# Performance work log

Hardware: AMD Instinct MI355X
Metric: run time of the kernel (lower is better)

The kernel has to match this reference:

```python
import jax, jax.numpy as jnp
import numpy as np
import math

B, N, D, H, T = 256, 512, 512, 8, 128
HD = D // H
CLIP = 10.0
CAP = 1.0
NEG = -1.0e9


def setup_inputs() -> dict:
    key = jax.random.key(0)
    ks = jax.random.split(key, 12)
    s = 1.0 / math.sqrt(D)
    return {
        "embeddings": jax.random.normal(ks[0], (B, N, D), jnp.float32),
        "mean_graph_emb": jax.random.normal(ks[1], (B, D), jnp.float32),
        "used_capacity": jax.random.uniform(ks[2], (T, B), jnp.float32),
        "Wk": jax.random.normal(ks[3], (D, D), jnp.float32) * s,
        "Wk_tanh": jax.random.normal(ks[4], (D, D), jnp.float32) * s,
        "Wv": jax.random.normal(ks[5], (D, D), jnp.float32) * s,
        "Wq_context": jax.random.normal(ks[6], (D, D), jnp.float32) * s,
        "Wq_step": jax.random.normal(ks[7], (D + 1, D), jnp.float32) * s,
        "Wout": jax.random.normal(ks[8], (D, D), jnp.float32) * s,
        "prev_a": jax.random.randint(ks[9], (T, B), 0, N, jnp.int32),
        "mask": jax.random.randint(ks[10], (T, B, N), 0, 2, jnp.int32),
    }


def reference(embeddings, mean_graph_emb, used_capacity, Wk, Wk_tanh, Wv,
              Wq_context, Wq_step, Wout, prev_a, mask):
    # Projections (done once per graph embedding, as in get_projections)
    K = (embeddings @ Wk).reshape(B, N, H, HD).transpose(0, 2, 1, 3)      # [B,H,N,hd]
    V = (embeddings @ Wv).reshape(B, N, H, HD).transpose(0, 2, 1, 3)      # [B,H,N,hd]
    K_tanh = embeddings @ Wk_tanh                                          # [B,N,D]
    Q_context = mean_graph_emb @ Wq_context                                # [B,D]

    inv_sqrt_hd = 1.0 / math.sqrt(HD)
    inv_sqrt_d = 1.0 / math.sqrt(D)

    def step(carry, xs):
        prev_t, cap_t, mask_t = xs  # [B], [B], [B,N]
        # get_step_context: gather prev node embedding + remaining capacity
        cur_emb = jnp.take_along_axis(embeddings, prev_t[:, None, None], axis=1)[:, 0]  # [B,D]
        step_ctx = jnp.concatenate([cur_emb, (CAP - cap_t)[:, None]], axis=-1)          # [B,D+1]
        q = Q_context + step_ctx @ Wq_step                                               # [B,D]
        qh = q.reshape(B, H, HD)                                                          # [B,H,hd]
        # decoder MHA, seq_len_q = 1
        logits = jnp.einsum("bhd,bhnd->bhn", qh, K) * inv_sqrt_hd                        # [B,H,N]
        logits = jnp.where(mask_t[:, None, :] == 1, NEG, logits)
        attn = jax.nn.softmax(logits, axis=-1)
        mha = jnp.einsum("bhn,bhnd->bhd", attn, V).reshape(B, D) @ Wout                  # [B,D]
        # single-head tanh-clipped pointer logits
        comp = jnp.einsum("bd,bnd->bn", mha, K_tanh) * inv_sqrt_d                        # [B,N]
        comp = jnp.tanh(comp) * CLIP
        comp = jnp.where(mask_t == 1, NEG, comp)
        p = jax.nn.softmax(comp, axis=-1)                                                # [B,N]
        return carry, p

    _, ps = jax.lax.scan(step, None, (prev_a, used_capacity, mask))  # [T,B,N]
    return ps.transpose(1, 0, 2)  # [B,T,N]
```

## Files before the change

### kernel.cpp

```cpp
#include <hip/hip_runtime.h>
#include <hip/hip_bf16.h>

constexpr int Bb = 256;
constexpr int Nn = 512;
constexpr int Dd = 512;
constexpr int Hh = 8;
constexpr int Tt = 128;
#define NEGF (-1.0e9f)

typedef __attribute__((ext_vector_type(4))) float f32x4;
typedef __attribute__((ext_vector_type(8))) short bf16x8;
typedef __attribute__((ext_vector_type(8))) unsigned short u16x8;

#define AS1 __attribute__((address_space(1)))
#define AS3 __attribute__((address_space(3)))

__device__ __forceinline__ unsigned short f2bf(float f) {
  union { float f; unsigned u; } v; v.f = f;
  unsigned r = v.u + 0x7fffu + ((v.u >> 16) & 1u);
  return (unsigned short)(r >> 16);
}

__device__ __forceinline__ unsigned cvtpk(float lo, float hi) {
  unsigned r;
  asm("v_cvt_pk_bf16_f32 %0, %1, %2" : "=v"(r) : "v"(lo), "v"(hi));
  return r;
}

__global__ void cast_emb_k(const float* __restrict__ src, unsigned short* __restrict__ dst, int n8) {
  int i = blockIdx.x * 256 + threadIdx.x;
  if (i >= n8) return;
  const float4* s = (const float4*)src + (size_t)i * 2;
  float4 a = s[0], b = s[1];
  u16x8 o;
  o[0] = f2bf(a.x); o[1] = f2bf(a.y); o[2] = f2bf(a.z); o[3] = f2bf(a.w);
  o[4] = f2bf(b.x); o[5] = f2bf(b.y); o[6] = f2bf(b.z); o[7] = f2bf(b.w);
  ((u16x8*)dst)[i] = o;
}

__global__ void cast_wt_k(const float* __restrict__ W0, const float* __restrict__ W1,
                          const float* __restrict__ W2,
                          unsigned short* __restrict__ D0, unsigned short* __restrict__ D1,
                          unsigned short* __restrict__ D2) {
  int mid = blockIdx.x >> 8;
  int tile = blockIdx.x & 255;
  const float* S = (mid == 0) ? W0 : (mid == 1) ? W1 : W2;
  unsigned short* Dst = (mid == 0) ? D0 : (mid == 1) ? D1 : D2;
  __shared__ float t[32][33];
  int r0 = (tile >> 4) * 32, c0 = (tile & 15) * 32;
  int tx = threadIdx.x & 31, ty = threadIdx.x >> 5;
#pragma unroll
  for (int yy = 0; yy < 4; ++yy) {
    int r = ty + yy * 8;
    t[r][tx] = S[(size_t)(r0 + r) * 512 + c0 + tx];
  }
  __syncthreads();
#pragma unroll
  for (int yy = 0; yy < 4; ++yy) {
    int c = ty + yy * 8;
    Dst[(size_t)(c0 + c) * 512 + r0 + tx] = f2bf(t[tx][c]);
  }
}

__global__ void qc_k(const float* __restrict__ mge, const float* __restrict__ Wqc,
                     float* __restrict__ Qc) {
  int b = blockIdx.x;
  __shared__ float m[512];
  m[threadIdx.x] = mge[(size_t)b * 512 + threadIdx.x];
  m[threadIdx.x + 256] = mge[(size_t)b * 512 + threadIdx.x + 256];
  __syncthreads();
  float a0 = 0.f, a1 = 0.f;
  for (int k = 0; k < 512; ++k) {
    float mk = m[k];
    a0 += mk * Wqc[(size_t)k * 512 + threadIdx.x];
    a1 += mk * Wqc[(size_t)k * 512 + threadIdx.x + 256];
  }
  Qc[(size_t)b * 512 + threadIdx.x] = a0;
  Qc[(size_t)b * 512 + threadIdx.x + 256] = a1;
}

__global__ void mbits_k(const int* __restrict__ mask, unsigned* __restrict__ bits) {
  size_t gid = (size_t)blockIdx.x * 256 + threadIdx.x;
  int mv = mask[gid];
  unsigned long long bal = __ballot(mv == 1);
  if ((threadIdx.x & 63) == 0) {
    unsigned t = (unsigned)(gid >> 17);
    unsigned b = (unsigned)((gid >> 9) & 255);
    unsigned n = (unsigned)(gid & 511);
    unsigned* dst = bits + (((size_t)b * 128 + t) * 16 + (n >> 5));
    dst[0] = (unsigned)bal;
    dst[1] = (unsigned)(bal >> 32);
  }
}

__device__ __forceinline__ void stage_tile(const unsigned short* __restrict__ G, int row0, int k0,
                                           unsigned short* lds_base, int wave, int lane) {
#pragma unroll
  for (int c = 0; c < 4; ++c) {
    int chunk = wave * 4 + c;
    const unsigned short* g = G + (size_t)(row0 + chunk * 8 + (lane >> 3)) * 512 + k0 + (lane & 7) * 8;
    __builtin_amdgcn_global_load_lds((AS1 void*)g, (AS3 void*)(lds_base + chunk * 512), 16, 0, 0);
  }
}

template <int MODE>
__global__ __launch_bounds__(256, 2)
void gemm5_k(const unsigned short* __restrict__ A, const unsigned short* __restrict__ BT,
             void* __restrict__ Cout,
             const float* __restrict__ Qc, const float* __restrict__ WqsL,
             const float* __restrict__ capp, const int* __restrict__ prev) {
  __shared__ __align__(16) char lds[32768];
  unsigned short* ldsA = (unsigned short*)lds;
  unsigned short* ldsB = ldsA + 8192;
  int xcd = blockIdx.x & 7, loc = blockIdx.x >> 3;
  int ml = loc >> 2, nt = loc & 3;
  int mt = xcd * 32 + ml;
  int m0 = mt * 128, n0 = nt * 128;
  int tid = threadIdx.x, lane = tid & 63, w = tid >> 6;
  int wm = w >> 1, wn = w & 1;
  int l15 = lane & 15, l4 = lane >> 4;

  const unsigned short* gbase[4];
#pragma unroll
  for (int c = 0; c < 4; ++c) {
    int row = m0 + (w * 4 + c) * 8 + (lane >> 3);
    if (MODE == 3) {
      int t = row >> 8, bb = row & 255;
      int pa = prev[t * Bb + bb];
      gbase[c] = A + (size_t)(bb * 512 + pa) * 512 + (lane & 7) * 8;
    } else {
      gbase[c] = A + (size_t)row * 512 + (lane & 7) * 8;
    }
  }

  f32x4 acc[4][4] = {};
  for (int k0 = 0; k0 < 512; k0 += 64) {
#pragma unroll
    for (int c = 0; c < 4; ++c) {
      int chunk = w * 4 + c;
      __builtin_amdgcn_global_load_lds((AS1 void*)(gbase[c] + k0),
                                       (AS3 void*)(ldsA + chunk * 512), 16, 0, 0);
    }
    stage_tile(BT, n0, k0, ldsB, w, lane);
    __syncthreads();
#pragma unroll
    for (int ks = 0; ks < 2; ++ks) {
      bf16x8 fa[4], fb[4];
#pragma unroll
      for (int ii = 0; ii < 4; ++ii)
        fa[ii] = *(const bf16x8*)(ldsA + (wm * 64 + ii * 16 + l15) * 64 + ks * 32 + l4 * 8);
#pragma unroll
      for (int jj = 0; jj < 4; ++jj)
        fb[jj] = *(const bf16x8*)(ldsB + (wn * 64 + jj * 16 + l15) * 64 + ks * 32 + l4 * 8);
#pragma unroll
      for (int ii = 0; ii < 4; ++ii)
#pragma unroll
        for (int jj = 0; jj < 4; ++jj)
          acc[ii][jj] = __builtin_amdgcn_mfma_f32_16x16x32_bf16(fa[ii], fb[jj], acc[ii][jj], 0, 0, 0);
    }
    __syncthreads();
  }

  if (MODE == 1) {
    unsigned short* C = (unsigned short*)Cout;
#pragma unroll
    for (int ii = 0; ii < 4; ++ii)
#pragma unroll
      for (int jj = 0; jj < 4; ++jj)
#pragma unroll
        for (int r = 0; r < 4; ++r) {
          int row = m0 + wm * 64 + ii * 16 + l4 * 4 + r;
          int col = n0 + wn * 64 + jj * 16 + l15;
          C[(size_t)row * 512 + col] = f2bf(acc[ii][jj][r]);
        }
  } else {
    unsigned short* C = (unsigned short*)Cout;
#pragma unroll
    for (int ii = 0; ii < 4; ++ii)
#pragma unroll
      for (int jj = 0; jj < 4; ++jj)
#pragma unroll
        for (int r = 0; r < 4; ++r) {
          int row = m0 + wm * 64 + ii * 16 + l4 * 4 + r;
          int col = n0 + wn * 64 + jj * 16 + l15;
          int t = row >> 8, bbx = row & 255;
          float val = acc[ii][jj][r] + Qc[(size_t)bbx * 512 + col] + (1.0f - capp[row]) * WqsL[col];
          C[(size_t)(bbx * 128 + t) * 512 + col] = f2bf(val * 0.125f);
        }
  }
}

__global__ __launch_bounds__(256, 2)
void wf_k(const unsigned short* __restrict__ A, const unsigned short* __restrict__ BT,
          unsigned short* __restrict__ C) {
  __shared__ __align__(16) char lds[32768];
  unsigned short* ldsA = (unsigned short*)lds;
  unsigned short* ldsB = ldsA + 8192;
  int mt = blockIdx.x >> 2, nt = blockIdx.x & 3;
  int m0 = mt * 128, n0 = nt * 128;
  int tid = threadIdx.x, lane = tid & 63, w = tid >> 6;
  int wm = w >> 1, wn = w & 1;
  int l15 = lane & 15, l4 = lane >> 4;

  f32x4 acc[4][4] = {};
  for (int k0 = 0; k0 < 512; k0 += 64) {
    stage_tile(A, m0, k0, ldsA, w, lane);
    stage_tile(BT, n0, k0, ldsB, w, lane);
    __syncthreads();
#pragma unroll
    for (int ks = 0; ks < 2; ++ks) {
      bf16x8 fa[4], fb[4];
#pragma unroll
      for (int ii = 0; ii < 4; ++ii)
        fa[ii] = *(const bf16x8*)(ldsA + (wm * 64 + ii * 16 + l15) * 64 + ks * 32 + l4 * 8);
#pragma unroll
      for (int jj = 0; jj < 4; ++jj)
        fb[jj] = *(const bf16x8*)(ldsB + (wn * 64 + jj * 16 + l15) * 64 + ks * 32 + l4 * 8);
#pragma unroll
      for (int ii = 0; ii < 4; ++ii)
#pragma unroll
        for (int jj = 0; jj < 4; ++jj)
          acc[ii][jj] = __builtin_amdgcn_mfma_f32_16x16x32_bf16(fa[ii], fb[jj], acc[ii][jj], 0, 0, 0);
    }
    __syncthreads();
  }
#pragma unroll
  for (int ii = 0; ii < 4; ++ii)
#pragma unroll
    for (int jj = 0; jj < 4; ++jj)
#pragma unroll
      for (int r = 0; r < 4; ++r) {
        int row = m0 + wm * 64 + ii * 16 + l4 * 4 + r;
        int col = n0 + wn * 64 + jj * 16 + l15;
        C[(size_t)row * 512 + col] = f2bf(acc[ii][jj][r]);
      }
}

#define STAGE10(SLOT, MAT, H, ROWB, KT)                                            \
  do {                                                                             \
    const unsigned short* G_ = (MAT) ? BT : A;                                     \
    int rb_ = (ROWB) + (H) * 128;                                                  \
    char* Lb_ = lds + (SLOT) * 65536 + (MAT) * 32768 + (H) * 16384;                \
    _Pragma("unroll")                                                              \
    for (int sh_ = 0; sh_ < 2; ++sh_) {                                            \
      int off_ = sh_ * 8192 + tid * 16;                                            \
      int r_ = off_ >> 7;                                                          \
      int c_ = (off_ & 127) ^ ((r_ & 7) << 4);     \
      const char* g_ = (const char*)(G_ + (size_t)(rb_ + r_) * 512 + (KT) * 64) + c_; \
      __builtin_amdgcn_global_load_lds((AS1 void*)g_, (AS3 void*)(Lb_ + off_), 16, 0, 0); \
    }                                                                              \
  } while (0)

#define LDA_Q(QM)                                                   \
  _Pragma("unroll")                                                 \
  for (int ii = 0; ii < 4; ++ii) {                                  \
    int rr_ = (QM) * 64 + ii * 16 + l15;                            \
    const char* ap_ = ldsAh + rr_ * 128;                            \
    int sw_ = (rr_ & 7) << 4;                                       \
    fa[ii][0] = *(const bf16x8*)(ap_ + ((l4 * 16) ^ sw_));          \
    fa[ii][1] = *(const bf16x8*)(ap_ + ((64 + l4 * 16) ^ sw_));     \
  }

#define LDB_Q(QN)                                                   \
  _Pragma("unroll")                                                 \
  for (int jj = 0; jj < 2; ++jj) {                                  \
    int rr_ = (wn & 1) * 64 + (QN) * 32 + jj * 16 + l15;            \
    const char* bp_ = ldsBh + rr_ * 128;                            \
    int sw_ = (rr_ & 7) << 4;                                       \
    fb[jj][0] = *(const bf16x8*)(bp_ + ((l4 * 16) ^ sw_));          \
    fb[jj][1] = *(const bf16x8*)(bp_ + ((64 + l4 * 16) ^ sw_));     \
  }

#define MM16(QM, QN)                                                              \
  do {                                                                            \
    __builtin_amdgcn_s_setprio(1);                                                \
    _Pragma("unroll")                                                             \
    for (int ii = 0; ii < 4; ++ii)                                                \
      _Pragma("unroll")                                                           \
      for (int jj = 0; jj < 2; ++jj) {                                            \
        acc[(QM) * 4 + ii][(QN) * 2 + jj] = __builtin_amdgcn_mfma_f32_16x16x32_bf16( \
            fa[ii][0], fb[jj][0], acc[(QM) * 4 + ii][(QN) * 2 + jj], 0, 0, 0);    \
        acc[(QM) * 4 + ii][(QN) * 2 + jj] = __builtin_amdgcn_mfma_f32_16x16x32_bf16( \
            fa[ii][1], fb[jj][1], acc[(QM) * 4 + ii][(QN) * 2 + jj], 0, 0, 0);    \
      }                                                                           \
    __builtin_amdgcn_s_setprio(0);                                                \
  } while (0)

__global__ __launch_bounds__(512, 1)
void gemm10_k(const unsigned short* __restrict__ A,
              const unsigned short* __restrict__ B0, const unsigned short* __restrict__ B1,
              unsigned short* __restrict__ C0, unsigned short* __restrict__ C2) {
  __shared__ __align__(16) char lds[131072];
  int xcd = blockIdx.x & 7, loc = blockIdx.x >> 3;
  int ml4 = loc >> 2, cmb = loc & 3;
  int grp = cmb >> 1, nh = cmb & 1;
  const unsigned short* BT = grp ? B1 : B0;
  int mtb = xcd * 64 + ml4 * 4;
  int n0 = nh * 256;
  int tid = threadIdx.x, lane = tid & 63, w = tid >> 6;
  int wm = w >> 2, wn = w & 3;
  int l15 = lane & 15, l4 = lane >> 4;

  f32x4 acc[8][4] = {};
  bf16x8 fa[4][2], fb[2][2];

  {
    int m0n = mtb * 256;
    STAGE10(0, 0, 0, m0n, 0); STAGE10(0, 0, 1, m0n, 0);
    STAGE10(0, 1, 0, n0, 0);  STAGE10(0, 1, 1, n0, 0);
  }

  for (int g = 0; g < 32; ++g) {
    int s = g & 1, sn = s ^ 1;
    char* ldsAh = lds + s * 65536 + wm * 16384;
    char* ldsBh = lds + s * 65536 + 32768 + (wn >> 1) * 16384;
    int gn = g + 1;
    int m0n = (mtb + (gn >> 3)) * 256;
    int ktn = gn & 7;
    if (g < 31) {
      STAGE10(sn, 0, 0, m0n, ktn);
      asm volatile("s_waitcnt vmcnt(2)" ::: "memory");
    } else {
      asm volatile("s_waitcnt vmcnt(0)" ::: "memory");
    }
    __builtin_amdgcn_s_barrier();
    LDA_Q(0); LDB_Q(0);
    MM16(0, 0);
    __builtin_amdgcn_s_barrier();
    LDB_Q(1);
    if (g < 31) STAGE10(sn, 0, 1, m0n, ktn);
    __builtin_amdgcn_s_barrier();
    MM16(0, 1);
    __builtin_amdgcn_s_barrier();
    LDA_Q(1);
    if (g < 31) STAGE10(sn, 1, 0, n0, ktn);
    __builtin_amdgcn_s_barrier();
    MM16(1, 1);
    __builtin_amdgcn_s_barrier();
    LDB_Q(0);
    if (g < 31) STAGE10(sn, 1, 1, n0, ktn);
    __builtin_amdgcn_s_barrier();
    MM16(1, 0);
    __builtin_amdgcn_s_barrier();

    if ((g & 7) == 7) {
      int m0cur = (mtb + (g >> 3)) * 256;
      if (grp == 0) {
#pragma unroll
        for (int mi = 0; mi < 8; ++mi)
#pragma unroll
          for (int nj = 0; nj < 4; ++nj)
#pragma unroll
            for (int r = 0; r < 4; ++r) {
              int row = m0cur + wm * 128 + mi * 16 + l4 * 4 + r;
              int col = n0 + wn * 64 + nj * 16 + l15;
              C0[(size_t)row * 512 + col] = f2bf(acc[mi][nj][r]);
            }
      } else {
        int bb = m0cur >> 9, nn0 = m0cur & 511;
        char* wb = lds + 65536 + w * 8192;
#pragma unroll
        for (int p = 0; p < 4; ++p) {
#pragma unroll
          for (int mi = 0; mi < 8; ++mi) {
            ushort4 w4;
            w4.x = f2bf(acc[mi][p][0]);
            w4.y = f2bf(acc[mi][p][1]);
            w4.z = f2bf(acc[mi][p][2]);
            w4.w = f2bf(acc[mi][p][3]);
            *(ushort4*)(wb + l15 * 264 + (mi * 16 + l4 * 4) * 2) = w4;
          }
#pragma unroll
          for (int step = 0; step < 4; ++step) {
            int dl = step * 4 + l4;
            union { ushort4 h[2]; u16x8 v; } u;
            u.h[0] = *(const ushort4*)(wb + dl * 264 + l15 * 16);
            u.h[1] = *(const ushort4*)(wb + dl * 264 + l15 * 16 + 8);
            int dglob = n0 + wn * 64 + p * 16 + dl;
            *(u16x8*)(C2 + (size_t)(bb * 512 + dglob) * 512 + nn0 + wm * 128 + l15 * 8) = u.v;
          }
        }
      }
#pragma unroll
      for (int mi = 0; mi < 8; ++mi)
#pragma unroll
        for (int nj = 0; nj < 4; ++nj)
          acc[mi][nj] = (f32x4){0.f, 0.f, 0.f, 0.f};
      __syncthreads();
    }
  }
}

#define STAGEK5(CH, SLOT)                                                          \
  do {                                                                             \
    _Pragma("unroll")                                                              \
    for (int sh_ = 0; sh_ < 2; ++sh_) {                                            \
      int off_ = sh_ * 8192 + tid * 16;                                            \
      int r_ = off_ >> 7;                                                          \
      int c_ = (off_ & 127) ^ ((r_ & 7) << 4);                                     \
      const char* g_ = (const char*)(Kb + (size_t)(b * 512 + (CH) * 128 + r_) * 512 + h * 64) + c_; \
      __builtin_amdgcn_global_load_lds((AS1 void*)g_, (AS3 void*)(lds + (SLOT) * 16384 + off_), 16, 0, 0); \
    }                                                                              \
  } while (0)

#define STAGEV5(CH, SLOT)                                                          \
  do {                                                                             \
    _Pragma("unroll")                                                              \
    for (int sh_ = 0; sh_ < 2; ++sh_) {                                            \
      int off_ = sh_ * 8192 + tid * 16;                                            \
      int r_ = off_ >> 8;                                                          \
      int c_ = (off_ & 255) ^ ((r_ & 7) << 4);                                     \
      const char* g_ = (const char*)(Vt + (size_t)(b * 512 + h * 64 + r_) * 512 + (CH) * 128) + c_; \
      __builtin_amdgcn_global_load_lds((AS1 void*)g_, (AS3 void*)(lds + 32768 + (SLOT) * 16384 + off_), 16, 0, 0); \
    }                                                                              \
  } while (0)

#define CHUNK5(CH)                                                                 \
  do {                                                                             \
    const char* Ks_ = lds + ((CH) & 1) * 16384;                                    \
    const char* Vs_ = lds + 32768 + ((CH) & 1) * 16384;                            \
    f32x4 sck[8];                                                                  \
    _Pragma("unroll")                                                              \
    for (int jj = 0; jj < 8; ++jj) sck[jj] = (f32x4){0.f, 0.f, 0.f, 0.f};          \
    _Pragma("unroll")                                                              \
    for (int jj = 0; jj < 8; ++jj) {                                               \
      int rr_ = jj * 16 + l15;                                                     \
      int sw_ = (rr_ & 7) << 4;                                                    \
      bf16x8 k0_ = *(const bf16x8*)(Ks_ + rr_ * 128 + ((l4 * 16) ^ sw_));          \
      bf16x8 k1_ = *(const bf16x8*)(Ks_ + rr_ * 128 + ((64 + l4 * 16) ^ sw_));     \
      sck[jj] = __builtin_amdgcn_mfma_f32_16x16x32_bf16(k0_, fq[0], sck[jj], 0, 0, 0); \
      sck[jj] = __builtin_amdgcn_mfma_f32_16x16x32_bf16(k1_, fq[1], sck[jj], 0, 0, 0); \
    }                                                                              \
    unsigned mwarr_[4] = {mqs[CH].x, mqs[CH].y, mqs[CH].z, mqs[CH].w};             \
    float cmx_ = -3.0e38f;                                                         \
    _Pragma("unroll")                                                              \
    for (int jj = 0; jj < 8; ++jj) {                                               \
      unsigned nib_ = mwarr_[jj >> 1] >> (((jj & 1) << 4) + (l4 << 2));            \
      _Pragma("unroll")                                                            \
      for (int r = 0; r < 4; ++r)                                                  \
        sck[jj][r] = ((nib_ >> r) & 1) ? NEGF : sck[jj][r];                        \
      float m01_ = fmaxf(sck[jj][0], sck[jj][1]);                                  \
      float m23_ = fmaxf(sck[jj][2], sck[jj][3]);                                  \
      cmx_ = fmaxf(cmx_, fmaxf(m01_, m23_));                                       \
    }                                                                              \
    cmx_ = fmaxf(cmx_, __shfl_xor(cmx_, 16));                                      \
    cmx_ = fmaxf(cmx_, __shfl_xor(cmx_, 32));                                      \
    float mn_ = fmaxf(mx, cmx_);                                                   \
    float al_ = __expf(mx - mn_);                                                  \
    sum *= al_;                                                                    \
    _Pragma("unroll")                                                              \
    for (int dj = 0; dj < 4; ++dj)                                                 \
      _Pragma("unroll")                                                            \
      for (int r = 0; r < 4; ++r) o[dj][r] *= al_;                                 \
    mx = mn_;                                                                      \
    _Pragma("unroll")                                                              \
    for (int jj = 0; jj < 8; ++jj) {                                               \
      _Pragma("unroll")                                                            \
      for (int r = 0; r < 4; ++r) sck[jj][r] = __expf(sck[jj][r] - mx);            \
      sum += (sck[jj][0] + sck[jj][1]) + (sck[jj][2] + sck[jj][3]);                \
    }                                                                              \
    _Pragma("unroll")                                                              \
    for (int g = 0; g < 4; ++g) {                                                  \
      unsigned a0_ = cvtpk(sck[2 * g][0], sck[2 * g][1]);                          \
      unsigned a1_ = cvtpk(sck[2 * g][2], sck[2 * g][3]);                          \
      unsigned b0_ = cvtpk(sck[2 * g + 1][0], sck[2 * g + 1][1]);                  \
      unsigned b1_ = cvtpk(sck[2 * g + 1][2], sck[2 * g + 1][3]);                  \
      unsigned wA0_ = __shfl(a0_, src0, 64), wB0_ = __shfl(b0_, src0, 64);         \
      unsigned wA1_ = __shfl(a1_, src0, 64), wB1_ = __shfl(b1_, src0, 64);         \
      unsigned wA2_ = __shfl(a0_, src2, 64), wB2_ = __shfl(b0_, src2, 64);         \
      unsigned wA3_ = __shfl(a1_, src2, 64), wB3_ = __shfl(b1_, src2, 64);         \
      union { unsigned u[4]; bf16x8 v; } pu_;                                      \
      pu_.u[0] = loh ? wA0_ : wB0_;                                                \
      pu_.u[1] = loh ? wA1_ : wB1_;                                                \
      pu_.u[2] = loh ? wA2_ : wB2_;                                                \
      pu_.u[3] = loh ? wA3_ : wB3_;                                                \
      _Pragma("unroll")                                                            \
      for (int dj = 0; dj < 4; ++dj) {                                             \
        int rr_ = dj * 16 + l15;                                                   \
        int sw_ = (rr_ & 7) << 4;                                                  \
        bf16x8 fv_ = *(const bf16x8*)(Vs_ + rr_ * 256 + ((g * 64 + l4 * 16) ^ sw_)); \
        o[dj] = __builtin_amdgcn_mfma_f32_16x16x32_bf16(fv_, pu_.v, o[dj], 0, 0, 0); \
      }                                                                            \
    }                                                                              \
  } while (0)

__global__ __launch_bounds__(512, 4)
void attn5_k(const unsigned short* __restrict__ Qb, const unsigned short* __restrict__ Kb,
             const unsigned short* __restrict__ Vt, const unsigned* __restrict__ mbits,
             unsigned short* __restrict__ mhaB) {
  __shared__ __align__(16) char lds[65536];
  int bid = blockIdx.x;
  int h = bid & 7, b = bid >> 3;
  int tid = threadIdx.x, lane = tid & 63, w = tid >> 6;
  int l15 = lane & 15, l4 = lane >> 4;
  int t = w * 16 + l15;

  bf16x8 fq[2];
#pragma unroll
  for (int ks = 0; ks < 2; ++ks)
    fq[ks] = *(const bf16x8*)(Qb + (size_t)(b * 128 + t) * 512 + h * 64 + ks * 32 + l4 * 8);
  uint4 mqs[4];
  {
    const uint4* mp = (const uint4*)(mbits + (((size_t)b * 128 + t) << 4));
    mqs[0] = mp[0]; mqs[1] = mp[1]; mqs[2] = mp[2]; mqs[3] = mp[3];
  }

  float mx = -3.0e38f, sum = 0.f;
  f32x4 o[4] = {};
  int src0 = l15 + ((l4 & 1) ? 32 : 0);
  int src2 = l15 + ((l4 & 1) ? 48 : 16);
  bool loh = (l4 < 2);

  STAGEK5(0, 0); STAGEV5(0, 0);
  STAGEK5(1, 1); STAGEV5(1, 1);
  asm volatile("s_waitcnt vmcnt(4)" ::: "memory");
  __builtin_amdgcn_s_barrier();
  CHUNK5(0);
  __builtin_amdgcn_s_barrier();
  STAGEK5(2, 0); STAGEV5(2, 0);
  asm volatile("s_waitcnt vmcnt(4)" ::: "memory");
  __builtin_amdgcn_s_barrier();
  CHUNK5(1);
  __builtin_amdgcn_s_barrier();
  STAGEK5(3, 1); STAGEV5(3, 1);
  asm volatile("s_waitcnt vmcnt(4)" ::: "memory");
  __builtin_amdgcn_s_barrier();
  CHUNK5(2);
  __builtin_amdgcn_s_barrier();
  asm volatile("s_waitcnt vmcnt(0)" ::: "memory");
  __builtin_amdgcn_s_barrier();
  CHUNK5(3);

  sum += __shfl_xor(sum, 16);
  sum += __shfl_xor(sum, 32);
  float inv = 1.0f / sum;
#pragma unroll
  for (int dj = 0; dj < 4; ++dj) {
    ushort4 w4;
    w4.x = f2bf(o[dj][0] * inv);
    w4.y = f2bf(o[dj][1] * inv);
    w4.z = f2bf(o[dj][2] * inv);
    w4.w = f2bf(o[dj][3] * inv);
    *(ushort4*)(mhaB + (size_t)(b * 128 + t) * 512 + h * 64 + dj * 16 + l4 * 4) = w4;
  }
}

#define STAGEC(CH, SLOT)                                                           \
  do {                                                                             \
    _Pragma("unroll")                                                              \
    for (int ps_ = 0; ps_ < 8; ++ps_) {                                            \
      int off_ = ps_ * 8192 + tid * 16;                                            \
      int r_ = off_ >> 10;                                                         \
      int c_ = (off_ & 1023) ^ ((r_ & 7) << 4);                                    \
      const char* g_ = (const char*)(embB + (size_t)(b * 512 + (CH) * 64 + r_) * 512) + c_; \
      __builtin_amdgcn_global_load_lds((AS1 void*)g_, (AS3 void*)(lds + (SLOT) * 65536 + off_), 16, 0, 0); \
    }                                                                              \
  } while (0)

#define CCHUNK(CH)                                                                 \
  do {                                                                             \
    const char* Es_ = lds + ((CH) & 1) * 65536;                                    \
    _Pragma("unroll")                                                              \
    for (int jjl_ = 0; jjl_ < 4; ++jjl_) {                                         \
      f32x4 sck = (f32x4){0.f, 0.f, 0.f, 0.f};                                     \
      int rr_ = jjl_ * 16 + l15;                                                   \
      const char* ep_ = Es_ + rr_ * 1024;                                          \
      int sw_ = (rr_ & 7) << 4;                                                    \
      _Pragma("unroll")                                                            \
      for (int ks_ = 0; ks_ < 16; ++ks_) {                                         \
        bf16x8 fa_ = *(const bf16x8*)(ep_ + ((ks_ * 64 + l4 * 16) ^ sw_));         \
        sck = __builtin_amdgcn_mfma_f32_16x16x32_bf16(fa_, fb[ks_], sck, 0, 0, 0); \
      }                                                                            \
      int jg_ = (CH) * 4 + jjl_;                                                   \
      unsigned nib_ = mw[jg_ >> 1] >> (((jg_ & 1) << 4) + (l4 << 2));              \
      float4 o4_;                                                                  \
      float* po_ = (float*)&o4_;                                                   \
      _Pragma("unroll")                                                            \
      for (int r = 0; r < 4; ++r) {                                                \
        float y_ = sck[r] * 0.044194173824159216f;                                 \
        y_ = fminf(fmaxf(y_, -15.f), 15.f);                                        \
        float e2_ = __expf(2.f * y_);                                              \
        float th_ = (e2_ - 1.f) / (e2_ + 1.f);                                     \
        float p_ = __expf(th_ * 10.f - 10.f);                                      \
        p_ = ((nib_ >> r) & 1) ? 0.f : p_;                                         \
        po_[r] = p_;                                                               \
        sum += p_;                                                                 \
      }                                                                            \
      *(float4*)(out + (size_t)(b * 128 + t) * 512 + (CH) * 64 + jjl_ * 16 + l4 * 4) = o4_; \
    }                                                                              \
  } while (0)

__global__ __launch_bounds__(512, 1)
void comp4_k(const unsigned short* __restrict__ mh2, const unsigned short* __restrict__ embB,
             const unsigned* __restrict__ mbits, float* __restrict__ out,
             float* __restrict__ sums) {
  __shared__ __align__(16) char lds[131072];
  int b = blockIdx.x;
  int tid = threadIdx.x, lane = tid & 63, w = tid >> 6;
  int l15 = lane & 15, l4 = lane >> 4;
  int t = w * 16 + l15;

  bf16x8 fb[16];
#pragma unroll
  for (int ks = 0; ks < 16; ++ks)
    fb[ks] = *(const bf16x8*)(mh2 + (size_t)(b * 128 + t) * 512 + ks * 32 + l4 * 8);
  unsigned mw[16];
  {
    const uint4* mp = (const uint4*)(mbits + (((size_t)b * 128 + t) << 4));
    uint4 a0 = mp[0], a1 = mp[1], a2 = mp[2], a3 = mp[3];
    mw[0] = a0.x; mw[1] = a0.y; mw[2] = a0.z; mw[3] = a0.w;
    mw[4] = a1.x; mw[5] = a1.y; mw[6] = a1.z; mw[7] = a1.w;
    mw[8] = a2.x; mw[9] = a2.y; mw[10] = a2.z; mw[11] = a2.w;
    mw[12] = a3.x; mw[13] = a3.y; mw[14] = a3.z; mw[15] = a3.w;
  }

  float sum = 0.f;
  STAGEC(0, 0);
  STAGEC(1, 1);
  asm volatile("s_waitcnt vmcnt(8)" ::: "memory");
  __builtin_amdgcn_s_barrier();
  CCHUNK(0);
  __builtin_amdgcn_s_barrier();
  STAGEC(2, 0);
  asm volatile("s_waitcnt vmcnt(8)" ::: "memory");
  __builtin_amdgcn_s_barrier();
  CCHUNK(1);
  __builtin_amdgcn_s_barrier();
  STAGEC(3, 1);
  asm volatile("s_waitcnt vmcnt(8)" ::: "memory");
  __builtin_amdgcn_s_barrier();
  CCHUNK(2);
  __builtin_amdgcn_s_barrier();
  STAGEC(4, 0);
  asm volatile("s_waitcnt vmcnt(8)" ::: "memory");
  __builtin_amdgcn_s_barrier();
  CCHUNK(3);
  __builtin_amdgcn_s_barrier();
  STAGEC(5, 1);
  asm volatile("s_waitcnt vmcnt(8)" ::: "memory");
  __builtin_amdgcn_s_barrier();
  CCHUNK(4);
  __builtin_amdgcn_s_barrier();
  STAGEC(6, 0);
  asm volatile("s_waitcnt vmcnt(8)" ::: "memory");
  __builtin_amdgcn_s_barrier();
  CCHUNK(5);
  __builtin_amdgcn_s_barrier();
  STAGEC(7, 1);
  asm volatile("s_waitcnt vmcnt(8)" ::: "memory");
  __builtin_amdgcn_s_barrier();
  CCHUNK(6);
  __builtin_amdgcn_s_barrier();
  asm volatile("s_waitcnt vmcnt(0)" ::: "memory");
  __builtin_amdgcn_s_barrier();
  CCHUNK(7);

  sum += __shfl_xor(sum, 16);
  sum += __shfl_xor(sum, 32);
  if (l4 == 0) sums[b * 128 + t] = sum;
}

__global__ void norm_k(float* __restrict__ out, const float* __restrict__ sums) {
  int row = blockIdx.x * 4 + (threadIdx.x >> 6);
  int lane = threadIdx.x & 63;
  float inv = 1.0f / sums[row];
  float4* p = (float4*)(out + (size_t)row * 512) + lane;
  float4 a = p[0], b = p[64];
  a.x *= inv; a.y *= inv; a.z *= inv; a.w *= inv;
  b.x *= inv; b.y *= inv; b.z *= inv; b.w *= inv;
  p[0] = a; p[64] = b;
}

extern "C" void kernel_launch(void* const* d_in, const int* in_sizes, int n_in,
                              void* d_out, int out_size, void* d_ws, size_t ws_size,
                              hipStream_t stream) {
  (void)in_sizes; (void)n_in; (void)out_size; (void)ws_size;
  const float* emb  = (const float*)d_in[0];
  const float* mge  = (const float*)d_in[1];
  const float* cap  = (const float*)d_in[2];
  const float* Wk   = (const float*)d_in[3];
  const float* Wkt  = (const float*)d_in[4];
  const float* Wv   = (const float*)d_in[5];
  const float* Wqc  = (const float*)d_in[6];
  const float* Wqs  = (const float*)d_in[7];
  const float* Wout = (const float*)d_in[8];
  const int* prev   = (const int*)d_in[9];
  const int* mask   = (const int*)d_in[10];
  float* out = (float*)d_out;

  char* p = (char*)d_ws;
  auto take = [&](size_t n) { char* q = p; p += (n + 255) & ~(size_t)255; return q; };
  unsigned short* embB = (unsigned short*)take((size_t)131072 * 512 * 2);
  unsigned short* Kb   = (unsigned short*)take((size_t)131072 * 512 * 2);
  unsigned short* Vt   = (unsigned short*)take((size_t)131072 * 512 * 2);
  unsigned short* Qb   = (unsigned short*)take((size_t)32768 * 512 * 2);
  unsigned short* mhaB = (unsigned short*)take((size_t)32768 * 512 * 2);
  unsigned short* mh2  = (unsigned short*)take((size_t)32768 * 512 * 2);
  float*          Qc   = (float*)take((size_t)256 * 512 * 4);
  unsigned*       mbit = (unsigned*)take((size_t)256 * 128 * 16 * 4);
  float*          sums = (float*)take((size_t)32768 * 4);
  unsigned short* WkT  = (unsigned short*)take(524288);
  unsigned short* WvT  = (unsigned short*)take(524288);
  unsigned short* WqsT = (unsigned short*)take(524288);
  unsigned short* WktB = (unsigned short*)take(524288);
  unsigned short* WoutB= (unsigned short*)take(524288);
  unsigned short* WFT  = (unsigned short*)take(524288);

  cast_emb_k<<<32768, 256, 0, stream>>>(emb, embB, 8388608);
  cast_emb_k<<<128, 256, 0, stream>>>(Wkt, WktB, 32768);
  cast_emb_k<<<128, 256, 0, stream>>>(Wout, WoutB, 32768);
  cast_wt_k<<<768, 256, 0, stream>>>(Wk, Wv, Wqs, WkT, WvT, WqsT);
  qc_k<<<256, 256, 0, stream>>>(mge, Wqc, Qc);
  mbits_k<<<65536, 256, 0, stream>>>(mask, mbit);
  wf_k<<<16, 256, 0, stream>>>(WktB, WoutB, WFT);
  gemm5_k<3><<<1024, 256, 0, stream>>>(embB, WqsT, Qb, Qc, Wqs + 512 * 512, cap, prev);
  gemm10_k<<<512, 512, 0, stream>>>(embB, WkT, WvT, Kb, Vt);
  attn5_k<<<2048, 512, 0, stream>>>(Qb, Kb, Vt, mbit, mhaB);
  gemm5_k<1><<<1024, 256, 0, stream>>>(mhaB, WFT, mh2, nullptr, nullptr, nullptr, nullptr);
  comp4_k<<<256, 512, 0, stream>>>(mh2, embB, mbit, out, sums);
  norm_k<<<8192, 256, 0, stream>>>(out, sums);
}
```

Measured before the change: 543.0 us.

## Split pointer-logit kernel over node halves and compute Q_context with MFMA GEMM

The pointer-logit kernel now runs two blocks per batch element, each covering half of the N nodes with half the LDS. Each block writes its own partial softmax sum, and the normalization kernel adds the two. This doubles the block count from 256 to 512 and allows two blocks per CU, so more of the machine is used. Separately, the scalar fp32 Q_context kernel is replaced by a bf16 MFMA small GEMM on cast inputs, which lowers that product's precision to bf16. A stray label 'wf_cast:' sits in the host function.

```diff
diff --git a/kernel.cpp b/kernel.cpp
--- a/kernel.cpp
+++ b/kernel.cpp
@@ -39,13 +39,13 @@
 }
 
 __global__ void cast_wt_k(const float* __restrict__ W0, const float* __restrict__ W1,
-                          const float* __restrict__ W2,
+                          const float* __restrict__ W2, const float* __restrict__ W3,
                           unsigned short* __restrict__ D0, unsigned short* __restrict__ D1,
-                          unsigned short* __restrict__ D2) {
+                          unsigned short* __restrict__ D2, unsigned short* __restrict__ D3) {
   int mid = blockIdx.x >> 8;
   int tile = blockIdx.x & 255;
-  const float* S = (mid == 0) ? W0 : (mid == 1) ? W1 : W2;
-  unsigned short* Dst = (mid == 0) ? D0 : (mid == 1) ? D1 : D2;
+  const float* S = (mid == 0) ? W0 : (mid == 1) ? W1 : (mid == 2) ? W2 : W3;
+  unsigned short* Dst = (mid == 0) ? D0 : (mid == 1) ? D1 : (mid == 2) ? D2 : D3;
   __shared__ float t[32][33];
   int r0 = (tile >> 4) * 32, c0 = (tile & 15) * 32;
   int tx = threadIdx.x & 31, ty = threadIdx.x >> 5;
@@ -60,23 +60,6 @@
     int c = ty + yy * 8;
     Dst[(size_t)(c0 + c) * 512 + r0 + tx] = f2bf(t[tx][c]);
   }
-}
-
-__global__ void qc_k(const float* __restrict__ mge, const float* __restrict__ Wqc,
-                     float* __restrict__ Qc) {
-  int b = blockIdx.x;
-  __shared__ float m[512];
-  m[threadIdx.x] = mge[(size_t)b * 512 + threadIdx.x];
-  m[threadIdx.x + 256] = mge[(size_t)b * 512 + threadIdx.x + 256];
-  __syncthreads();
-  float a0 = 0.f, a1 = 0.f;
-  for (int k = 0; k < 512; ++k) {
-    float mk = m[k];
-    a0 += mk * Wqc[(size_t)k * 512 + threadIdx.x];
-    a1 += mk * Wqc[(size_t)k * 512 + threadIdx.x + 256];
-  }
-  Qc[(size_t)b * 512 + threadIdx.x] = a0;
-  Qc[(size_t)b * 512 + threadIdx.x + 256] = a1;
 }
 
 __global__ void mbits_k(const int* __restrict__ mask, unsigned* __restrict__ bits) {
@@ -190,9 +173,10 @@
   }
 }
 
+template <int OUTF>
 __global__ __launch_bounds__(256, 2)
-void wf_k(const unsigned short* __restrict__ A, const unsigned short* __restrict__ BT,
-          unsigned short* __restrict__ C) {
+void smallgemm_k(const unsigned short* __restrict__ A, const unsigned short* __restrict__ BT,
+                 void* __restrict__ Cout) {
   __shared__ __align__(16) char lds[32768];
   unsigned short* ldsA = (unsigned short*)lds;
   unsigned short* ldsB = ldsA + 8192;
@@ -232,7 +216,8 @@
       for (int r = 0; r < 4; ++r) {
         int row = m0 + wm * 64 + ii * 16 + l4 * 4 + r;
         int col = n0 + wn * 64 + jj * 16 + l15;
-        C[(size_t)row * 512 + col] = f2bf(acc[ii][jj][r]);
+        if (OUTF) ((float*)Cout)[(size_t)row * 512 + col] = acc[ii][jj][r];
+        else ((unsigned short*)Cout)[(size_t)row * 512 + col] = f2bf(acc[ii][jj][r]);
       }
 }
 
@@ -545,23 +530,23 @@
   }
 }
 
-#define STAGEC(CH, SLOT)                                                           \
+#define STAGEC5(CH, SLOT)                                                          \
   do {                                                                             \
     _Pragma("unroll")                                                              \
-    for (int ps_ = 0; ps_ < 8; ++ps_) {                                            \
+    for (int ps_ = 0; ps_ < 4; ++ps_) {                                            \
       int off_ = ps_ * 8192 + tid * 16;                                            \
       int r_ = off_ >> 10;                                                         \
       int c_ = (off_ & 1023) ^ ((r_ & 7) << 4);                                    \
-      const char* g_ = (const char*)(embB + (size_t)(b * 512 + (CH) * 64 + r_) * 512) + c_; \
-      __builtin_amdgcn_global_load_lds((AS1 void*)g_, (AS3 void*)(lds + (SLOT) * 65536 + off_), 16, 0, 0); \
+      const char* g_ = (const char*)(embB + (size_t)(b * 512 + nh * 256 + (CH) * 32 + r_) * 512) + c_; \
+      __builtin_amdgcn_global_load_lds((AS1 void*)g_, (AS3 void*)(lds + (SLOT) * 32768 + off_), 16, 0, 0); \
     }                                                                              \
   } while (0)
 
-#define CCHUNK(CH)                                                                 \
+#define CCHUNK5(CH)                                                                \
   do {                                                                             \
-    const char* Es_ = lds + ((CH) & 1) * 65536;                                    \
-    _Pragma("unroll")                                                              \
-    for (int jjl_ = 0; jjl_ < 4; ++jjl_) {                                         \
+    const char* Es_ = lds + ((CH) & 1) * 32768;                                    \
+    _Pragma("unroll")                                                              \
+    for (int jjl_ = 0; jjl_ < 2; ++jjl_) {                                         \
       f32x4 sck = (f32x4){0.f, 0.f, 0.f, 0.f};                                     \
       int rr_ = jjl_ * 16 + l15;                                                   \
       const char* ep_ = Es_ + rr_ * 1024;                                          \
@@ -571,8 +556,7 @@
         bf16x8 fa_ = *(const bf16x8*)(ep_ + ((ks_ * 64 + l4 * 16) ^ sw_));         \
         sck = __builtin_amdgcn_mfma_f32_16x16x32_bf16(fa_, fb[ks_], sck, 0, 0, 0); \
       }                                                                            \
-      int jg_ = (CH) * 4 + jjl_;                                                   \
-      unsigned nib_ = mw[jg_ >> 1] >> (((jg_ & 1) << 4) + (l4 << 2));              \
+      unsigned nib_ = mwh[CH] >> ((jjl_ << 4) + (l4 << 2));                        \
       float4 o4_;                                                                  \
       float* po_ = (float*)&o4_;                                                   \
       _Pragma("unroll")                                                            \
@@ -586,16 +570,16 @@
         po_[r] = p_;                                                               \
         sum += p_;                                                                 \
       }                                                                            \
-      *(float4*)(out + (size_t)(b * 128 + t) * 512 + (CH) * 64 + jjl_ * 16 + l4 * 4) = o4_; \
+      *(float4*)(out + (size_t)(b * 128 + t) * 512 + nh * 256 + (CH) * 32 + jjl_ * 16 + l4 * 4) = o4_; \
     }                                                                              \
   } while (0)
 
-__global__ __launch_bounds__(512, 1)
-void comp4_k(const unsigned short* __restrict__ mh2, const unsigned short* __restrict__ embB,
+__global__ __launch_bounds__(512, 2)
+void comp5_k(const unsigned short* __restrict__ mh2, const unsigned short* __restrict__ embB,
              const unsigned* __restrict__ mbits, float* __restrict__ out,
              float* __restrict__ sums) {
-  __shared__ __align__(16) char lds[131072];
-  int b = blockIdx.x;
+  __shared__ __align__(16) char lds[65536];
+  int b = blockIdx.x >> 1, nh = blockIdx.x & 1;
   int tid = threadIdx.x, lane = tid & 63, w = tid >> 6;
   int l15 = lane & 15, l4 = lane >> 4;
   int t = w * 16 + l15;
@@ -604,66 +588,64 @@
 #pragma unroll
   for (int ks = 0; ks < 16; ++ks)
     fb[ks] = *(const bf16x8*)(mh2 + (size_t)(b * 128 + t) * 512 + ks * 32 + l4 * 8);
-  unsigned mw[16];
+  unsigned mwh[8];
   {
-    const uint4* mp = (const uint4*)(mbits + (((size_t)b * 128 + t) << 4));
-    uint4 a0 = mp[0], a1 = mp[1], a2 = mp[2], a3 = mp[3];
-    mw[0] = a0.x; mw[1] = a0.y; mw[2] = a0.z; mw[3] = a0.w;
-    mw[4] = a1.x; mw[5] = a1.y; mw[6] = a1.z; mw[7] = a1.w;
-    mw[8] = a2.x; mw[9] = a2.y; mw[10] = a2.z; mw[11] = a2.w;
-    mw[12] = a3.x; mw[13] = a3.y; mw[14] = a3.z; mw[15] = a3.w;
+    const uint4* mp = (const uint4*)(mbits + (((size_t)b * 128 + t) << 4)) + nh * 2;
+    uint4 a0 = mp[0], a1 = mp[1];
+    mwh[0] = a0.x; mwh[1] = a0.y; mwh[2] = a0.z; mwh[3] = a0.w;
+    mwh[4] = a1.x; mwh[5] = a1.y; mwh[6] = a1.z; mwh[7] = a1.w;
   }
 
   float sum = 0.f;
-  STAGEC(0, 0);
-  STAGEC(1, 1);
-  asm volatile("s_waitcnt vmcnt(8)" ::: "memory");
-  __builtin_amdgcn_s_barrier();
-  CCHUNK(0);
-  __builtin_amdgcn_s_barrier();
-  STAGEC(2, 0);
-  asm volatile("s_waitcnt vmcnt(8)" ::: "memory");
-  __builtin_amdgcn_s_barrier();
-  CCHUNK(1);
-  __builtin_amdgcn_s_barrier();
-  STAGEC(3, 1);
-  asm volatile("s_waitcnt vmcnt(8)" ::: "memory");
-  __builtin_amdgcn_s_barrier();
-  CCHUNK(2);
-  __builtin_amdgcn_s_barrier();
-  STAGEC(4, 0);
-  asm volatile("s_waitcnt vmcnt(8)" ::: "memory");
-  __builtin_amdgcn_s_barrier();
-  CCHUNK(3);
-  __builtin_amdgcn_s_barrier();
-  STAGEC(5, 1);
-  asm volatile("s_waitcnt vmcnt(8)" ::: "memory");
-  __builtin_amdgcn_s_barrier();
-  CCHUNK(4);
-  __builtin_amdgcn_s_barrier();
-  STAGEC(6, 0);
-  asm volatile("s_waitcnt vmcnt(8)" ::: "memory");
-  __builtin_amdgcn_s_barrier();
-  CCHUNK(5);
-  __builtin_amdgcn_s_barrier();
-  STAGEC(7, 1);
-  asm volatile("s_waitcnt vmcnt(8)" ::: "memory");
-  __builtin_amdgcn_s_barrier();
-  CCHUNK(6);
+  STAGEC5(0, 0);
+  STAGEC5(1, 1);
+  asm volatile("s_waitcnt vmcnt(4)" ::: "memory");
+  __builtin_amdgcn_s_barrier();
+  CCHUNK5(0);
+  __builtin_amdgcn_s_barrier();
+  STAGEC5(2, 0);
+  asm volatile("s_waitcnt vmcnt(4)" ::: "memory");
+  __builtin_amdgcn_s_barrier();
+  CCHUNK5(1);
+  __builtin_amdgcn_s_barrier();
+  STAGEC5(3, 1);
+  asm volatile("s_waitcnt vmcnt(4)" ::: "memory");
+  __builtin_amdgcn_s_barrier();
+  CCHUNK5(2);
+  __builtin_amdgcn_s_barrier();
+  STAGEC5(4, 0);
+  asm volatile("s_waitcnt vmcnt(4)" ::: "memory");
+  __builtin_amdgcn_s_barrier();
+  CCHUNK5(3);
+  __builtin_amdgcn_s_barrier();
+  STAGEC5(5, 1);
+  asm volatile("s_waitcnt vmcnt(4)" ::: "memory");
+  __builtin_amdgcn_s_barrier();
+  CCHUNK5(4);
+  __builtin_amdgcn_s_barrier();
+  STAGEC5(6, 0);
+  asm volatile("s_waitcnt vmcnt(4)" ::: "memory");
+  __builtin_amdgcn_s_barrier();
+  CCHUNK5(5);
+  __builtin_amdgcn_s_barrier();
+  STAGEC5(7, 1);
+  asm volatile("s_waitcnt vmcnt(4)" ::: "memory");
+  __builtin_amdgcn_s_barrier();
+  CCHUNK5(6);
   __builtin_amdgcn_s_barrier();
   asm volatile("s_waitcnt vmcnt(0)" ::: "memory");
   __builtin_amdgcn_s_barrier();
-  CCHUNK(7);
+  CCHUNK5(7);
 
   sum += __shfl_xor(sum, 16);
   sum += __shfl_xor(sum, 32);
-  if (l4 == 0) sums[b * 128 + t] = sum;
+  if (l4 == 0) sums[nh * 32768 + b * 128 + t] = sum;
 }
 
 __global__ void norm_k(float* __restrict__ out, const float* __restrict__ sums) {
   int row = blockIdx.x * 4 + (threadIdx.x >> 6);
   int lane = threadIdx.x & 63;
-  float inv = 1.0f / sums[row];
+  float inv = 1.0f / (sums[row] + sums[32768 + row]);
   float4* p = (float4*)(out + (size_t)row * 512) + lane;
   float4 a = p[0], b = p[64];
   a.x *= inv; a.y *= inv; a.z *= inv; a.w *= inv;
@@ -698,25 +680,29 @@
   unsigned short* mh2  = (unsigned short*)take((size_t)32768 * 512 * 2);
   float*          Qc   = (float*)take((size_t)256 * 512 * 4);
   unsigned*       mbit = (unsigned*)take((size_t)256 * 128 * 16 * 4);
-  float*          sums = (float*)take((size_t)32768 * 4);
+  float*          sums = (float*)take((size_t)2 * 32768 * 4);
   unsigned short* WkT  = (unsigned short*)take(524288);
   unsigned short* WvT  = (unsigned short*)take(524288);
   unsigned short* WqsT = (unsigned short*)take(524288);
+  unsigned short* WqcT = (unsigned short*)take(524288);
   unsigned short* WktB = (unsigned short*)take(524288);
   unsigned short* WoutB= (unsigned short*)take(524288);
   unsigned short* WFT  = (unsigned short*)take(524288);
+  unsigned short* mgeB = (unsigned short*)take((size_t)256 * 512 * 2);
 
   cast_emb_k<<<32768, 256, 0, stream>>>(emb, embB, 8388608);
   cast_emb_k<<<128, 256, 0, stream>>>(Wkt, WktB, 32768);
   cast_emb_k<<<128, 256, 0, stream>>>(Wout, WoutB, 32768);
-  cast_wt_k<<<768, 256, 0, stream>>>(Wk, Wv, Wqs, WkT, WvT, WqsT);
-  qc_k<<<256, 256, 0, stream>>>(mge, Wqc, Qc);
+  cast_emb_k<<<64, 256, 0, stream>>>(mge, mgeB, 16384);
+  cast_wt_k<<<1024, 256, 0, stream>>>(Wk, Wv, Wqs, Wqc, WkT, WvT, WqsT, WqcT);
   mbits_k<<<65536, 256, 0, stream>>>(mask, mbit);
-  wf_k<<<16, 256, 0, stream>>>(WktB, WoutB, WFT);
+  wf_cast:
+  smallgemm_k<0><<<16, 256, 0, stream>>>(WktB, WoutB, WFT);
+  smallgemm_k<1><<<8, 256, 0, stream>>>(mgeB, WqcT, Qc);
   gemm5_k<3><<<1024, 256, 0, stream>>>(embB, WqsT, Qb, Qc, Wqs + 512 * 512, cap, prev);
   gemm10_k<<<512, 512, 0, stream>>>(embB, WkT, WvT, Kb, Vt);
   attn5_k<<<2048, 512, 0, stream>>>(Qb, Kb, Vt, mbit, mhaB);
   gemm5_k<1><<<1024, 256, 0, stream>>>(mhaB, WFT, mh2, nullptr, nullptr, nullptr, nullptr);
-  comp4_k<<<256, 512, 0, stream>>>(mh2, embB, mbit, out, sums);
+  comp5_k<<<512, 512, 0, stream>>>(mh2, embB, mbit, out, sums);
   norm_k<<<8192, 256, 0, stream>>>(out, sums);
 }
```

Result: no change. 534.8 us (-1.5%).
